# Kernel tuning notes

Measured on AMD Instinct MI355X. Metric: run time of the kernel, lower is better.

## Reference

```python
import jax, jax.numpy as jnp
import numpy as np

GAMMA = 0.1
EPS = 1e-10


def setup_inputs() -> dict:
    key = jax.random.key(0)
    ks = jax.random.split(key, 7)
    B, N, D = 1024, 2048, 128
    return {
        "target_embed": jax.random.normal(ks[0], (B, D), dtype=jnp.float32),
        "candidate_embeds": jax.random.normal(ks[1], (B, N, D), dtype=jnp.float32),
        "Wq": jax.random.normal(ks[2], (D, D), dtype=jnp.float32) * 0.05,
        "bq": jax.random.normal(ks[3], (D,), dtype=jnp.float32) * 0.05,
        "Wk": jax.random.normal(ks[4], (D, D), dtype=jnp.float32) * 0.05,
        "bk": jax.random.normal(ks[5], (D,), dtype=jnp.float32) * 0.05,
        "u": jax.random.uniform(ks[6], (B, N), dtype=jnp.float32),
        "num_neighbors": 32,
    }


def reference(target_embed, candidate_embeds, Wq, bq, Wk, bk, u, num_neighbors):
    B, N, D = candidate_embeds.shape
    scale = jnp.sqrt(jnp.float32(D))
    # Linear projections (torch Linear: x @ W.T + b)
    Q = target_embed @ Wq.T + bq                      # [B, D]
    K = jnp.einsum('bnd,ed->bne', candidate_embeds, Wk) + bk  # [B, N, D]
    scores = jnp.einsum('bd,bnd->bn', Q, K) / scale   # [B, N]
    p = jax.nn.softmax(scores, axis=-1)
    p = (1.0 - GAMMA) * p + GAMMA / N                 # mix with uniform
    # multinomial without replacement == Gumbel top-k on log-probs
    gumbel = -jnp.log(-jnp.log(u + EPS) + EPS)        # [B, N]
    _, sampled_idx = jax.lax.top_k(jnp.log(p) + gumbel, num_neighbors)  # [B, k]
    return sampled_idx
```

## Files before the change

### kernel.cpp

```cpp
#include <hip/hip_runtime.h>
#include <cmath>
#include <cfloat>
#include <climits>

constexpr int D    = 128;
constexpr float EPS_ = 1e-10f;
constexpr int KMAX = 64;

__global__ __launch_bounds__(128) void proj_kernel(
    const float* __restrict__ target, const float* __restrict__ Wq,
    const float* __restrict__ bq, const float* __restrict__ Wk,
    float* __restrict__ qt)
{
  __shared__ float sTgt[D];
  __shared__ float sQ[D];
  const int b = blockIdx.x, tid = threadIdx.x;
  sTgt[tid] = target[(size_t)b * D + tid];
  __syncthreads();
  float acc = 0.f;
  const float* wrow = Wq + (size_t)tid * D;
  #pragma unroll 8
  for (int e = 0; e < D; ++e) acc += sTgt[e] * wrow[e];
  sQ[tid] = acc + bq[tid];
  __syncthreads();
  acc = 0.f;
  #pragma unroll 8
  for (int d = 0; d < D; ++d) acc += sQ[d] * Wk[(size_t)d * D + tid];
  qt[(size_t)b * D + tid] = acc;
}

constexpr int NT1 = 256;
__global__ __launch_bounds__(NT1, 8) void score_kernel(
    const float* __restrict__ cand, const float* __restrict__ qt,
    float* __restrict__ scores, int N, int rows_per_blk)
{
  const int b    = blockIdx.x;
  const int tid  = threadIdx.x;
  const int lane = tid & 63;
  const int wave = tid >> 6;
  const int grp  = lane >> 4;
  const int gl   = lane & 15;

  const float* qp = qt + (size_t)b * D + gl * 8;
  float4 qa = ((const float4*)qp)[0];
  float4 qb = ((const float4*)qp)[1];

  const float scale = sqrtf((float)D);
  const int n0 = blockIdx.y * rows_per_blk;
  const int n1 = n0 + rows_per_blk;
  const float* base = cand + (size_t)b * N * D;
  float* srow = scores + (size_t)b * N;

  for (int n = n0 + wave * 4 + grp; n < n1; n += 32) {
    const float4* r0 = (const float4*)(base + (size_t)n * D);
    const float4* r1 = (const float4*)(base + (size_t)(n + 16) * D);
    float4 a0 = r0[gl * 2 + 0];
    float4 a1 = r0[gl * 2 + 1];
    float4 c0 = r1[gl * 2 + 0];
    float4 c1 = r1[gl * 2 + 1];
    float p0 = a0.x * qa.x + a0.y * qa.y + a0.z * qa.z + a0.w * qa.w
             + a1.x * qb.x + a1.y * qb.y + a1.z * qb.z + a1.w * qb.w;
    float p1 = c0.x * qa.x + c0.y * qa.y + c0.z * qa.z + c0.w * qa.w
             + c1.x * qb.x + c1.y * qb.y + c1.z * qb.z + c1.w * qb.w;
    p0 += __shfl_xor(p0, 1);  p1 += __shfl_xor(p1, 1);
    p0 += __shfl_xor(p0, 2);  p1 += __shfl_xor(p1, 2);
    p0 += __shfl_xor(p0, 4);  p1 += __shfl_xor(p1, 4);
    p0 += __shfl_xor(p0, 8);  p1 += __shfl_xor(p1, 8);
    if (gl == 0) { srow[n] = p0 / scale; srow[n + 16] = p1 / scale; }
  }
}

constexpr int NT2 = 256;
__global__ __launch_bounds__(NT2) void topk_kernel(
    const float* __restrict__ scores, const float* __restrict__ u,
    const int* __restrict__ kptr, int* __restrict__ out, int N)
{
  __shared__ float redM[4];
  __shared__ float redS[4];
  __shared__ float cV[4 * KMAX];
  __shared__ int   cI[4 * KMAX];

  const int b    = blockIdx.x;
  const int tid  = threadIdx.x;
  const int lane = tid & 63;
  const int wave = tid >> 6;
  const int base = wave * 512 + lane * 8;

  const float* srow = scores + (size_t)b * N;
  float4 s0 = ((const float4*)(srow + base))[0];
  float4 s1 = ((const float4*)(srow + base))[1];
  float v[8] = { s0.x, s0.y, s0.z, s0.w, s1.x, s1.y, s1.z, s1.w };

  float m = v[0];
  #pragma unroll
  for (int j = 1; j < 8; ++j) m = fmaxf(m, v[j]);
  for (int s = 32; s; s >>= 1) m = fmaxf(m, __shfl_xor(m, s));
  if (lane == 0) redM[wave] = m;
  __syncthreads();
  m = fmaxf(fmaxf(redM[0], redM[1]), fmaxf(redM[2], redM[3]));

  float ssum = 0.f;
  #pragma unroll
  for (int j = 0; j < 8; ++j) ssum += expf(v[j] - m);
  for (int s = 32; s; s >>= 1) ssum += __shfl_xor(ssum, s);
  if (lane == 0) redS[wave] = ssum;
  __syncthreads();
  const float Z = redS[0] + redS[1] + redS[2] + redS[3];

  const float mixc = (float)(0.1 / (double)N);
  const float* urow = u + (size_t)b * N;
  float4 u0 = ((const float4*)(urow + base))[0];
  float4 u1 = ((const float4*)(urow + base))[1];
  float uu[8] = { u0.x, u0.y, u0.z, u0.w, u1.x, u1.y, u1.z, u1.w };
  #pragma unroll
  for (int j = 0; j < 8; ++j) {
    float pmix = 0.9f * (expf(v[j] - m) / Z) + mixc;
    float g = -logf(-logf(uu[j] + EPS_) + EPS_);
    v[j] = logf(pmix) + g;
  }

  const int k = kptr[0];

  for (int i = 0; i < k; ++i) {
    float bv = v[0]; int bj = 0;
    #pragma unroll
    for (int j = 1; j < 8; ++j) if (v[j] > bv) { bv = v[j]; bj = j; }
    int bidx = base + bj;
    for (int s = 32; s; s >>= 1) {
      float ov = __shfl_xor(bv, s);
      int   oi = __shfl_xor(bidx, s);
      if (ov > bv || (ov == bv && oi < bidx)) { bv = ov; bidx = oi; }
    }
    if (lane == ((bidx - wave * 512) >> 3)) {
      int off = bidx & 7;
      #pragma unroll
      for (int j = 0; j < 8; ++j) if (off == j) v[j] = -FLT_MAX;
    }
    if (lane == 0) { cV[wave * KMAX + i] = bv; cI[wave * KMAX + i] = bidx; }
  }
  __syncthreads();

  if (wave == 0) {
    const int tot = 4 * k;
    float mv[4]; int mi[4];
    #pragma unroll
    for (int t = 0; t < 4; ++t) {
      int c = lane + 64 * t;
      if (c < tot) {
        int w = c / k, i = c % k;
        mv[t] = cV[w * KMAX + i]; mi[t] = cI[w * KMAX + i];
      } else { mv[t] = -FLT_MAX; mi[t] = INT_MAX; }
    }
    for (int i = 0; i < k; ++i) {
      float bv = mv[0]; int bidx = mi[0];
      #pragma unroll
      for (int t = 1; t < 4; ++t)
        if (mv[t] > bv || (mv[t] == bv && mi[t] < bidx)) { bv = mv[t]; bidx = mi[t]; }
      for (int s = 32; s; s >>= 1) {
        float ov = __shfl_xor(bv, s);
        int   oi = __shfl_xor(bidx, s);
        if (ov > bv || (ov == bv && oi < bidx)) { bv = ov; bidx = oi; }
      }
      #pragma unroll
      for (int t = 0; t < 4; ++t) if (mi[t] == bidx) mv[t] = -FLT_MAX;
      if (lane == 0) out[(size_t)b * k + i] = bidx;
    }
  }
}

constexpr int NTF = 512;
constexpr int NWF = NTF / 64;
__global__ __launch_bounds__(NTF, 8) void fused_kernel(
    const float* __restrict__ target, const float* __restrict__ cand,
    const float* __restrict__ Wq, const float* __restrict__ bq,
    const float* __restrict__ Wk, const float* __restrict__ u,
    const int* __restrict__ kptr, int* __restrict__ out, int N)
{
  extern __shared__ float sS[];
  __shared__ float sTgt[D];
  __shared__ float sQ[D];
  __shared__ float sQt[D];
  __shared__ float redV[NWF];
  __shared__ int   redI[NWF];

  const int b = blockIdx.x, tid = threadIdx.x;
  const int lane = tid & 63, wave = tid >> 6;

  if (tid < D) sTgt[tid] = target[(size_t)b * D + tid];
  __syncthreads();
  if (tid < D) {
    float acc = 0.f;
    const float* wrow = Wq + (size_t)tid * D;
    #pragma unroll 8
    for (int e = 0; e < D; ++e) acc += sTgt[e] * wrow[e];
    sQ[tid] = acc + bq[tid];
  }
  __syncthreads();
  if (tid < D) {
    float acc = 0.f;
    #pragma unroll 8
    for (int d = 0; d < D; ++d) acc += sQ[d] * Wk[(size_t)d * D + tid];
    sQt[tid] = acc;
  }
  __syncthreads();

  const int grp = lane >> 4, gl = lane & 15;
  float q0 = sQt[gl*8+0], q1 = sQt[gl*8+1], q2 = sQt[gl*8+2], q3 = sQt[gl*8+3];
  float q4 = sQt[gl*8+4], q5 = sQt[gl*8+5], q6 = sQt[gl*8+6], q7 = sQt[gl*8+7];
  const float scale = sqrtf((float)D);
  const int rstride = NWF * 4;
  int n = wave * 4 + grp;
  for (; n + rstride < N; n += 2 * rstride) {
    const float4* r0 = (const float4*)(cand + ((size_t)b * N + n) * D);
    const float4* r1 = (const float4*)(cand + ((size_t)b * N + n + rstride) * D);
    float4 a0 = r0[gl*2+0], a1 = r0[gl*2+1], c0 = r1[gl*2+0], c1 = r1[gl*2+1];
    float p0 = a0.x*q0 + a0.y*q1 + a0.z*q2 + a0.w*q3 + a1.x*q4 + a1.y*q5 + a1.z*q6 + a1.w*q7;
    float p1 = c0.x*q0 + c0.y*q1 + c0.z*q2 + c0.w*q3 + c1.x*q4 + c1.y*q5 + c1.z*q6 + c1.w*q7;
    p0 += __shfl_xor(p0,1); p1 += __shfl_xor(p1,1);
    p0 += __shfl_xor(p0,2); p1 += __shfl_xor(p1,2);
    p0 += __shfl_xor(p0,4); p1 += __shfl_xor(p1,4);
    p0 += __shfl_xor(p0,8); p1 += __shfl_xor(p1,8);
    if (gl == 0) { sS[n] = p0 / scale; sS[n + rstride] = p1 / scale; }
  }
  if (n < N) {
    const float4* r0 = (const float4*)(cand + ((size_t)b * N + n) * D);
    float4 a0 = r0[gl*2+0], a1 = r0[gl*2+1];
    float p0 = a0.x*q0 + a0.y*q1 + a0.z*q2 + a0.w*q3 + a1.x*q4 + a1.y*q5 + a1.z*q6 + a1.w*q7;
    p0 += __shfl_xor(p0,1); p0 += __shfl_xor(p0,2); p0 += __shfl_xor(p0,4); p0 += __shfl_xor(p0,8);
    if (gl == 0) sS[n] = p0 / scale;
  }
  __syncthreads();

  float m = -FLT_MAX;
  for (int i = tid; i < N; i += NTF) m = fmaxf(m, sS[i]);
  for (int s = 32; s; s >>= 1) m = fmaxf(m, __shfl_xor(m, s));
  if (lane == 0) redV[wave] = m;
  __syncthreads();
  m = redV[0];
  #pragma unroll
  for (int w = 1; w < NWF; ++w) m = fmaxf(m, redV[w]);
  __syncthreads();

  float ssum = 0.f;
  for (int i = tid; i < N; i += NTF) ssum += expf(sS[i] - m);
  for (int s = 32; s; s >>= 1) ssum += __shfl_xor(ssum, s);
  if (lane == 0) redV[wave] = ssum;
  __syncthreads();
  float Z = redV[0];
  #pragma unroll
  for (int w = 1; w < NWF; ++w) Z += redV[w];
  __syncthreads();

  const float mixc = (float)(0.1 / (double)N);
  for (int i = tid; i < N; i += NTF) {
    float pmix = 0.9f * (expf(sS[i] - m) / Z) + mixc;
    float uv = u[(size_t)b * N + i];
    float g = -logf(-logf(uv + EPS_) + EPS_);
    sS[i] = logf(pmix) + g;
  }
  __syncthreads();

  const int k = kptr[0];
  for (int i = 0; i < k; ++i) {
    float bv = -FLT_MAX; int bi = N;
    for (int j = tid; j < N; j += NTF) {
      float vv = sS[j];
      if (vv > bv || (vv == bv && j < bi)) { bv = vv; bi = j; }
    }
    for (int s = 32; s; s >>= 1) {
      float ov = __shfl_xor(bv, s); int oi = __shfl_xor(bi, s);
      if (ov > bv || (ov == bv && oi < bi)) { bv = ov; bi = oi; }
    }
    if (lane == 0) { redV[wave] = bv; redI[wave] = bi; }
    __syncthreads();
    if (tid == 0) {
      float fv = redV[0]; int fi = redI[0];
      #pragma unroll
      for (int w = 1; w < NWF; ++w)
        if (redV[w] > fv || (redV[w] == fv && redI[w] < fi)) { fv = redV[w]; fi = redI[w]; }
      out[(size_t)b * k + i] = fi;
      sS[fi] = -FLT_MAX;
    }
    __syncthreads();
  }
}

extern "C" void kernel_launch(void* const* d_in, const int* in_sizes, int n_in,
                              void* d_out, int out_size, void* d_ws, size_t ws_size,
                              hipStream_t stream) {
  const float* target = (const float*)d_in[0];
  const float* cand   = (const float*)d_in[1];
  const float* Wq     = (const float*)d_in[2];
  const float* bq     = (const float*)d_in[3];
  const float* Wk     = (const float*)d_in[4];
  const float* bk     = (const float*)d_in[5];
  const float* u      = (const float*)d_in[6];
  const int*   kptr   = (const int*)d_in[7];
  (void)bk; (void)n_in;

  const int B = in_sizes[0] / D;
  const int N = in_sizes[1] / (B * D);
  const int k = out_size / B;

  const size_t need = ((size_t)B * N + (size_t)B * D) * sizeof(float);
  const bool ok3 = (ws_size >= need) && (N == NT2 * 8) && (k <= KMAX) &&
                   (N % 128 == 0);

  if (ok3) {
    float* scores = (float*)d_ws;
    float* qt     = scores + (size_t)B * N;
    proj_kernel<<<B, 128, 0, stream>>>(target, Wq, bq, Wk, qt);
    const int chunks = 4;
    const int rows_per_blk = N / chunks;
    score_kernel<<<dim3(B, chunks), NT1, 0, stream>>>(cand, qt, scores, N, rows_per_blk);
    topk_kernel<<<B, NT2, 0, stream>>>(scores, u, kptr, (int*)d_out, N);
  } else {
    fused_kernel<<<B, NTF, N * sizeof(float), stream>>>(
        target, cand, Wq, bq, Wk, u, kptr, (int*)d_out, N);
  }
}
```

Before: 271.1 us.

## Fuse projection, scoring and top-k into one kernel per batch row

Replaces the three-kernel path (projection, score, top-k) with a single 512-thread kernel per batch row. Scores stay in shared memory instead of round-tripping through a global workspace, which removes two kernel launches and the score write and read-back. The candidate read now maps one float4 per lane with two rows per wave instruction. The cost is one block per row (1024 blocks) where scoring previously used four blocks per row, so there is less parallelism for the bandwidth-bound candidate stream. The projection also redoes the two 128x128 matvecs inside each block with only 128 of 512 threads active.

```diff
diff --git a/kernel.cpp b/kernel.cpp
--- a/kernel.cpp
+++ b/kernel.cpp
@@ -4,147 +4,141 @@
 #include <climits>
 
 constexpr int D    = 128;
+constexpr int NT   = 512;
+constexpr int NW   = NT / 64;
+constexpr int KMAX = 64;
 constexpr float EPS_ = 1e-10f;
-constexpr int KMAX = 64;
-
-__global__ __launch_bounds__(128) void proj_kernel(
-    const float* __restrict__ target, const float* __restrict__ Wq,
-    const float* __restrict__ bq, const float* __restrict__ Wk,
-    float* __restrict__ qt)
+
+__global__ __launch_bounds__(NT, 8) void fused2_kernel(
+    const float* __restrict__ target, const float* __restrict__ cand,
+    const float* __restrict__ Wq, const float* __restrict__ bq,
+    const float* __restrict__ Wk, const float* __restrict__ u,
+    const int* __restrict__ kptr, int* __restrict__ out, int N)
 {
-  __shared__ float sTgt[D];
-  __shared__ float sQ[D];
-  const int b = blockIdx.x, tid = threadIdx.x;
-  sTgt[tid] = target[(size_t)b * D + tid];
-  __syncthreads();
-  float acc = 0.f;
-  const float* wrow = Wq + (size_t)tid * D;
-  #pragma unroll 8
-  for (int e = 0; e < D; ++e) acc += sTgt[e] * wrow[e];
-  sQ[tid] = acc + bq[tid];
-  __syncthreads();
-  acc = 0.f;
-  #pragma unroll 8
-  for (int d = 0; d < D; ++d) acc += sQ[d] * Wk[(size_t)d * D + tid];
-  qt[(size_t)b * D + tid] = acc;
-}
-
-constexpr int NT1 = 256;
-__global__ __launch_bounds__(NT1, 8) void score_kernel(
-    const float* __restrict__ cand, const float* __restrict__ qt,
-    float* __restrict__ scores, int N, int rows_per_blk)
-{
+  extern __shared__ __align__(16) float sS[];
+  __shared__ __align__(16) float sTgt[D];
+  __shared__ __align__(16) float sQ[D];
+  __shared__ __align__(16) float sQt[D];
+  __shared__ float redM[NW];
+  __shared__ float cV[NW * KMAX];
+  __shared__ int   cI[NW * KMAX];
+
   const int b    = blockIdx.x;
   const int tid  = threadIdx.x;
   const int lane = tid & 63;
   const int wave = tid >> 6;
-  const int grp  = lane >> 4;
-  const int gl   = lane & 15;
-
-  const float* qp = qt + (size_t)b * D + gl * 8;
-  float4 qa = ((const float4*)qp)[0];
-  float4 qb = ((const float4*)qp)[1];
-
-  const float scale = sqrtf((float)D);
-  const int n0 = blockIdx.y * rows_per_blk;
-  const int n1 = n0 + rows_per_blk;
+
+  if (tid < D) sTgt[tid] = target[(size_t)b * D + tid];
+  __syncthreads();
+  if (tid < D) {
+    float acc = 0.f;
+    const float* wrow = Wq + (size_t)tid * D;
+    #pragma unroll 8
+    for (int e = 0; e < D; ++e) acc += sTgt[e] * wrow[e];
+    sQ[tid] = acc + bq[tid];
+  }
+  __syncthreads();
+  if (tid < D) {
+    float acc = 0.f;
+    #pragma unroll 8
+    for (int d = 0; d < D; ++d) acc += sQ[d] * Wk[(size_t)d * D + tid];
+    sQt[tid] = acc;
+  }
+  __syncthreads();
+
+  const int p    = lane & 31;
+  const int half = lane >> 5;
+  const float4 qf = ((const float4*)sQt)[p];
+  const float inv_scale = 1.0f / sqrtf((float)D);
   const float* base = cand + (size_t)b * N * D;
-  float* srow = scores + (size_t)b * N;
-
-  for (int n = n0 + wave * 4 + grp; n < n1; n += 32) {
-    const float4* r0 = (const float4*)(base + (size_t)n * D);
-    const float4* r1 = (const float4*)(base + (size_t)(n + 16) * D);
-    float4 a0 = r0[gl * 2 + 0];
-    float4 a1 = r0[gl * 2 + 1];
-    float4 c0 = r1[gl * 2 + 0];
-    float4 c1 = r1[gl * 2 + 1];
-    float p0 = a0.x * qa.x + a0.y * qa.y + a0.z * qa.z + a0.w * qa.w
-             + a1.x * qb.x + a1.y * qb.y + a1.z * qb.z + a1.w * qb.w;
-    float p1 = c0.x * qa.x + c0.y * qa.y + c0.z * qa.z + c0.w * qa.w
-             + c1.x * qb.x + c1.y * qb.y + c1.z * qb.z + c1.w * qb.w;
-    p0 += __shfl_xor(p0, 1);  p1 += __shfl_xor(p1, 1);
-    p0 += __shfl_xor(p0, 2);  p1 += __shfl_xor(p1, 2);
-    p0 += __shfl_xor(p0, 4);  p1 += __shfl_xor(p1, 4);
-    p0 += __shfl_xor(p0, 8);  p1 += __shfl_xor(p1, 8);
-    if (gl == 0) { srow[n] = p0 / scale; srow[n + 16] = p1 / scale; }
-  }
-}
-
-constexpr int NT2 = 256;
-__global__ __launch_bounds__(NT2) void topk_kernel(
-    const float* __restrict__ scores, const float* __restrict__ u,
-    const int* __restrict__ kptr, int* __restrict__ out, int N)
-{
-  __shared__ float redM[4];
-  __shared__ float redS[4];
-  __shared__ float cV[4 * KMAX];
-  __shared__ int   cI[4 * KMAX];
-
-  const int b    = blockIdx.x;
-  const int tid  = threadIdx.x;
-  const int lane = tid & 63;
-  const int wave = tid >> 6;
-  const int base = wave * 512 + lane * 8;
-
-  const float* srow = scores + (size_t)b * N;
-  float4 s0 = ((const float4*)(srow + base))[0];
-  float4 s1 = ((const float4*)(srow + base))[1];
-  float v[8] = { s0.x, s0.y, s0.z, s0.w, s1.x, s1.y, s1.z, s1.w };
-
-  float m = v[0];
-  #pragma unroll
-  for (int j = 1; j < 8; ++j) m = fmaxf(m, v[j]);
+
+  for (int n0 = wave * 8; n0 < N; n0 += NW * 8) {
+    const float4* r0 = (const float4*)(base + (size_t)(n0 + 0) * D) + lane;
+    const float4* r1 = (const float4*)(base + (size_t)(n0 + 2) * D) + lane;
+    const float4* r2 = (const float4*)(base + (size_t)(n0 + 4) * D) + lane;
+    const float4* r3 = (const float4*)(base + (size_t)(n0 + 6) * D) + lane;
+    float4 a0 = *r0, a1 = *r1, a2 = *r2, a3 = *r3;
+    float s0 = a0.x * qf.x + a0.y * qf.y + a0.z * qf.z + a0.w * qf.w;
+    float s1 = a1.x * qf.x + a1.y * qf.y + a1.z * qf.z + a1.w * qf.w;
+    float s2 = a2.x * qf.x + a2.y * qf.y + a2.z * qf.z + a2.w * qf.w;
+    float s3 = a3.x * qf.x + a3.y * qf.y + a3.z * qf.z + a3.w * qf.w;
+    s0 += __shfl_xor(s0, 1);  s1 += __shfl_xor(s1, 1);
+    s2 += __shfl_xor(s2, 1);  s3 += __shfl_xor(s3, 1);
+    s0 += __shfl_xor(s0, 2);  s1 += __shfl_xor(s1, 2);
+    s2 += __shfl_xor(s2, 2);  s3 += __shfl_xor(s3, 2);
+    s0 += __shfl_xor(s0, 4);  s1 += __shfl_xor(s1, 4);
+    s2 += __shfl_xor(s2, 4);  s3 += __shfl_xor(s3, 4);
+    s0 += __shfl_xor(s0, 8);  s1 += __shfl_xor(s1, 8);
+    s2 += __shfl_xor(s2, 8);  s3 += __shfl_xor(s3, 8);
+    s0 += __shfl_xor(s0, 16); s1 += __shfl_xor(s1, 16);
+    s2 += __shfl_xor(s2, 16); s3 += __shfl_xor(s3, 16);
+    if (p == 0) {
+      sS[n0 + 0 + half] = s0 * inv_scale;
+      sS[n0 + 2 + half] = s1 * inv_scale;
+      sS[n0 + 4 + half] = s2 * inv_scale;
+      sS[n0 + 6 + half] = s3 * inv_scale;
+    }
+  }
+  __syncthreads();
+
+  const int iv = wave * 256 + lane * 4;
+  float4 sv = *(const float4*)(sS + iv);
+  float v0 = sv.x, v1 = sv.y, v2 = sv.z, v3 = sv.w;
+
+  float m = fmaxf(fmaxf(v0, v1), fmaxf(v2, v3));
   for (int s = 32; s; s >>= 1) m = fmaxf(m, __shfl_xor(m, s));
   if (lane == 0) redM[wave] = m;
   __syncthreads();
-  m = fmaxf(fmaxf(redM[0], redM[1]), fmaxf(redM[2], redM[3]));
-
-  float ssum = 0.f;
+  m = redM[0];
   #pragma unroll
-  for (int j = 0; j < 8; ++j) ssum += expf(v[j] - m);
+  for (int w = 1; w < NW; ++w) m = fmaxf(m, redM[w]);
+  __syncthreads();
+
+  float ssum = expf(v0 - m) + expf(v1 - m) + expf(v2 - m) + expf(v3 - m);
   for (int s = 32; s; s >>= 1) ssum += __shfl_xor(ssum, s);
-  if (lane == 0) redS[wave] = ssum;
-  __syncthreads();
-  const float Z = redS[0] + redS[1] + redS[2] + redS[3];
+  if (lane == 0) redM[wave] = ssum;
+  __syncthreads();
+  float Z = redM[0];
+  #pragma unroll
+  for (int w = 1; w < NW; ++w) Z += redM[w];
+  __syncthreads();
 
   const float mixc = (float)(0.1 / (double)N);
-  const float* urow = u + (size_t)b * N;
-  float4 u0 = ((const float4*)(urow + base))[0];
-  float4 u1 = ((const float4*)(urow + base))[1];
-  float uu[8] = { u0.x, u0.y, u0.z, u0.w, u1.x, u1.y, u1.z, u1.w };
-  #pragma unroll
-  for (int j = 0; j < 8; ++j) {
-    float pmix = 0.9f * (expf(v[j] - m) / Z) + mixc;
-    float g = -logf(-logf(uu[j] + EPS_) + EPS_);
-    v[j] = logf(pmix) + g;
-  }
+  float4 uv = *(const float4*)(u + (size_t)b * N + iv);
+  v0 = logf(0.9f * (expf(v0 - m) / Z) + mixc) + (-logf(-logf(uv.x + EPS_) + EPS_));
+  v1 = logf(0.9f * (expf(v1 - m) / Z) + mixc) + (-logf(-logf(uv.y + EPS_) + EPS_));
+  v2 = logf(0.9f * (expf(v2 - m) / Z) + mixc) + (-logf(-logf(uv.z + EPS_) + EPS_));
+  v3 = logf(0.9f * (expf(v3 - m) / Z) + mixc) + (-logf(-logf(uv.w + EPS_) + EPS_));
 
   const int k = kptr[0];
 
   for (int i = 0; i < k; ++i) {
-    float bv = v[0]; int bj = 0;
-    #pragma unroll
-    for (int j = 1; j < 8; ++j) if (v[j] > bv) { bv = v[j]; bj = j; }
-    int bidx = base + bj;
+    float bv = v0; int bj = 0;
+    if (v1 > bv) { bv = v1; bj = 1; }
+    if (v2 > bv) { bv = v2; bj = 2; }
+    if (v3 > bv) { bv = v3; bj = 3; }
+    int bidx = iv + bj;
     for (int s = 32; s; s >>= 1) {
       float ov = __shfl_xor(bv, s);
       int   oi = __shfl_xor(bidx, s);
       if (ov > bv || (ov == bv && oi < bidx)) { bv = ov; bidx = oi; }
     }
-    if (lane == ((bidx - wave * 512) >> 3)) {
-      int off = bidx & 7;
-      #pragma unroll
-      for (int j = 0; j < 8; ++j) if (off == j) v[j] = -FLT_MAX;
+    if (lane == ((bidx & 255) >> 2)) {
+      int off = bidx & 3;
+      if (off == 0) v0 = -FLT_MAX;
+      if (off == 1) v1 = -FLT_MAX;
+      if (off == 2) v2 = -FLT_MAX;
+      if (off == 3) v3 = -FLT_MAX;
     }
     if (lane == 0) { cV[wave * KMAX + i] = bv; cI[wave * KMAX + i] = bidx; }
   }
   __syncthreads();
 
   if (wave == 0) {
-    const int tot = 4 * k;
-    float mv[4]; int mi[4];
+    const int tot = NW * k;
+    float mv[8]; int mi[8];
     #pragma unroll
-    for (int t = 0; t < 4; ++t) {
+    for (int t = 0; t < 8; ++t) {
       int c = lane + 64 * t;
       if (c < tot) {
         int w = c / k, i = c % k;
@@ -154,7 +148,7 @@
     for (int i = 0; i < k; ++i) {
       float bv = mv[0]; int bidx = mi[0];
       #pragma unroll
-      for (int t = 1; t < 4; ++t)
+      for (int t = 1; t < 8; ++t)
         if (mv[t] > bv || (mv[t] == bv && mi[t] < bidx)) { bv = mv[t]; bidx = mi[t]; }
       for (int s = 32; s; s >>= 1) {
         float ov = __shfl_xor(bv, s);
@@ -162,7 +156,7 @@
         if (ov > bv || (ov == bv && oi < bidx)) { bv = ov; bidx = oi; }
       }
       #pragma unroll
-      for (int t = 0; t < 4; ++t) if (mi[t] == bidx) mv[t] = -FLT_MAX;
+      for (int t = 0; t < 8; ++t) if (mi[t] == bidx) mv[t] = -FLT_MAX;
       if (lane == 0) out[(size_t)b * k + i] = bidx;
     }
   }
@@ -254,8 +248,8 @@
   const float mixc = (float)(0.1 / (double)N);
   for (int i = tid; i < N; i += NTF) {
     float pmix = 0.9f * (expf(sS[i] - m) / Z) + mixc;
-    float uv = u[(size_t)b * N + i];
-    float g = -logf(-logf(uv + EPS_) + EPS_);
+    float uvs = u[(size_t)b * N + i];
+    float g = -logf(-logf(uvs + EPS_) + EPS_);
     sS[i] = logf(pmix) + g;
   }
   __syncthreads();
@@ -296,24 +290,15 @@
   const float* bk     = (const float*)d_in[5];
   const float* u      = (const float*)d_in[6];
   const int*   kptr   = (const int*)d_in[7];
-  (void)bk; (void)n_in;
+  (void)bk; (void)n_in; (void)d_ws; (void)ws_size;
 
   const int B = in_sizes[0] / D;
   const int N = in_sizes[1] / (B * D);
   const int k = out_size / B;
 
-  const size_t need = ((size_t)B * N + (size_t)B * D) * sizeof(float);
-  const bool ok3 = (ws_size >= need) && (N == NT2 * 8) && (k <= KMAX) &&
-                   (N % 128 == 0);
-
-  if (ok3) {
-    float* scores = (float*)d_ws;
-    float* qt     = scores + (size_t)B * N;
-    proj_kernel<<<B, 128, 0, stream>>>(target, Wq, bq, Wk, qt);
-    const int chunks = 4;
-    const int rows_per_blk = N / chunks;
-    score_kernel<<<dim3(B, chunks), NT1, 0, stream>>>(cand, qt, scores, N, rows_per_blk);
-    topk_kernel<<<B, NT2, 0, stream>>>(scores, u, kptr, (int*)d_out, N);
+  if (N == NT * 4 && (N % 64) == 0 && k <= KMAX) {
+    fused2_kernel<<<B, NT, N * sizeof(float), stream>>>(
+        target, cand, Wq, bq, Wk, u, kptr, (int*)d_out, N);
   } else {
     fused_kernel<<<B, NTF, N * sizeof(float), stream>>>(
         target, cand, Wq, bq, Wk, u, kptr, (int*)d_out, N);
```

After: 246.3 us. 1.1x faster.

## Restructure score kernel with nontemporal loads, DPP reductions and double-buffered slots

Applied to the files above, without the earlier changes.

The score kernel now runs two blocks per batch row instead of four. Each wave processes 8-row slots, with each half-wave reducing one row through DPP row operations in place of shuffles. Candidate loads are nontemporal and double-buffered so the next slot's loads are in flight while the current one is reduced. A per-block rotation of the slot order spreads memory access. The aim is to stream the 1 GB candidate tensor closer to HBM bandwidth, at the cost of hardcoding N=2048, since the chunk and slot constants assume 1024 rows per block.

```diff
diff --git a/kernel.cpp b/kernel.cpp
--- a/kernel.cpp
+++ b/kernel.cpp
@@ -4,8 +4,28 @@
 #include <climits>
 
 constexpr int D    = 128;
+constexpr int KMAX = 64;
 constexpr float EPS_ = 1e-10f;
-constexpr int KMAX = 64;
+
+typedef float vf4 __attribute__((ext_vector_type(4)));
+__device__ __forceinline__ float4 ntload(const float4* p) {
+  vf4 v = __builtin_nontemporal_load((const vf4*)p);
+  return make_float4(v.x, v.y, v.z, v.w);
+}
+
+template <int CTRL>
+__device__ __forceinline__ float dpp_add(float x) {
+  int y = __builtin_amdgcn_update_dpp(0, __float_as_int(x), CTRL, 0xf, 0xf, false);
+  return x + __int_as_float(y);
+}
+__device__ __forceinline__ float dpp_sum32(float x) {
+  x = dpp_add<0x111>(x);
+  x = dpp_add<0x112>(x);
+  x = dpp_add<0x114>(x);
+  x = dpp_add<0x118>(x);
+  x = dpp_add<0x142>(x);
+  return x;
+}
 
 __global__ __launch_bounds__(128) void proj_kernel(
     const float* __restrict__ target, const float* __restrict__ Wq,
@@ -29,44 +49,75 @@
   qt[(size_t)b * D + tid] = acc;
 }
 
-constexpr int NT1 = 256;
-__global__ __launch_bounds__(NT1, 8) void score_kernel(
+__global__ __launch_bounds__(256) void score_kernel(
     const float* __restrict__ cand, const float* __restrict__ qt,
-    float* __restrict__ scores, int N, int rows_per_blk)
+    float* __restrict__ scores, int N)
 {
-  const int b    = blockIdx.x;
-  const int tid  = threadIdx.x;
-  const int lane = tid & 63;
-  const int wave = tid >> 6;
-  const int grp  = lane >> 4;
-  const int gl   = lane & 15;
-
-  const float* qp = qt + (size_t)b * D + gl * 8;
-  float4 qa = ((const float4*)qp)[0];
-  float4 qb = ((const float4*)qp)[1];
-
-  const float scale = sqrtf((float)D);
-  const int n0 = blockIdx.y * rows_per_blk;
-  const int n1 = n0 + rows_per_blk;
-  const float* base = cand + (size_t)b * N * D;
-  float* srow = scores + (size_t)b * N;
-
-  for (int n = n0 + wave * 4 + grp; n < n1; n += 32) {
-    const float4* r0 = (const float4*)(base + (size_t)n * D);
-    const float4* r1 = (const float4*)(base + (size_t)(n + 16) * D);
-    float4 a0 = r0[gl * 2 + 0];
-    float4 a1 = r0[gl * 2 + 1];
-    float4 c0 = r1[gl * 2 + 0];
-    float4 c1 = r1[gl * 2 + 1];
-    float p0 = a0.x * qa.x + a0.y * qa.y + a0.z * qa.z + a0.w * qa.w
-             + a1.x * qb.x + a1.y * qb.y + a1.z * qb.z + a1.w * qb.w;
-    float p1 = c0.x * qa.x + c0.y * qa.y + c0.z * qa.z + c0.w * qa.w
-             + c1.x * qb.x + c1.y * qb.y + c1.z * qb.z + c1.w * qb.w;
-    p0 += __shfl_xor(p0, 1);  p1 += __shfl_xor(p1, 1);
-    p0 += __shfl_xor(p0, 2);  p1 += __shfl_xor(p1, 2);
-    p0 += __shfl_xor(p0, 4);  p1 += __shfl_xor(p1, 4);
-    p0 += __shfl_xor(p0, 8);  p1 += __shfl_xor(p1, 8);
-    if (gl == 0) { srow[n] = p0 / scale; srow[n + 16] = p1 / scale; }
+  const int bid   = blockIdx.x;
+  const int b     = bid >> 1;
+  const int chunk = bid & 1;
+  const int tid   = threadIdx.x;
+  const int lane  = tid & 63;
+  const int wave  = tid >> 6;
+  const int p     = lane & 31;
+  const int half  = lane >> 5;
+
+  const float4 qf = ((const float4*)(qt + (size_t)b * D))[p];
+  const float inv_scale = 1.0f / sqrtf((float)D);
+
+  const float4* cb4 = (const float4*)(cand + (size_t)b * N * D) +
+                      (size_t)chunk * 1024 * 32;
+  float* srow = scores + (size_t)b * N + chunk * 1024;
+
+  constexpr int SLOTS = 128;
+  constexpr int ITERS = SLOTS / 4;
+  const int rot = (bid * 53) & (SLOTS - 1);
+
+  int slotA = (wave + rot) & (SLOTS - 1);
+  const float4* pA = cb4 + (size_t)slotA * 256 + lane;
+  float4 A0 = ntload(pA), A1 = ntload(pA + 64), A2 = ntload(pA + 128), A3 = ntload(pA + 192);
+
+  for (int i = 0; i < ITERS; i += 2) {
+    const int slotB = (wave + 4 * (i + 1) + rot) & (SLOTS - 1);
+    const float4* pB = cb4 + (size_t)slotB * 256 + lane;
+    float4 B0 = ntload(pB), B1 = ntload(pB + 64), B2 = ntload(pB + 128), B3 = ntload(pB + 192);
+
+    {
+      float s0 = A0.x * qf.x + A0.y * qf.y + A0.z * qf.z + A0.w * qf.w;
+      float s1 = A1.x * qf.x + A1.y * qf.y + A1.z * qf.z + A1.w * qf.w;
+      float s2 = A2.x * qf.x + A2.y * qf.y + A2.z * qf.z + A2.w * qf.w;
+      float s3 = A3.x * qf.x + A3.y * qf.y + A3.z * qf.z + A3.w * qf.w;
+      s0 = dpp_sum32(s0); s1 = dpp_sum32(s1); s2 = dpp_sum32(s2); s3 = dpp_sum32(s3);
+      if (p == 31) {
+        const int n0 = slotA * 8;
+        srow[n0 + 0 + half] = s0 * inv_scale;
+        srow[n0 + 2 + half] = s1 * inv_scale;
+        srow[n0 + 4 + half] = s2 * inv_scale;
+        srow[n0 + 6 + half] = s3 * inv_scale;
+      }
+    }
+
+    const int slotA2 = (wave + 4 * (i + 2) + rot) & (SLOTS - 1);
+    if (i + 2 < ITERS) {
+      const float4* pA2 = cb4 + (size_t)slotA2 * 256 + lane;
+      A0 = ntload(pA2); A1 = ntload(pA2 + 64); A2 = ntload(pA2 + 128); A3 = ntload(pA2 + 192);
+    }
+
+    {
+      float s0 = B0.x * qf.x + B0.y * qf.y + B0.z * qf.z + B0.w * qf.w;
+      float s1 = B1.x * qf.x + B1.y * qf.y + B1.z * qf.z + B1.w * qf.w;
+      float s2 = B2.x * qf.x + B2.y * qf.y + B2.z * qf.z + B2.w * qf.w;
+      float s3 = B3.x * qf.x + B3.y * qf.y + B3.z * qf.z + B3.w * qf.w;
+      s0 = dpp_sum32(s0); s1 = dpp_sum32(s1); s2 = dpp_sum32(s2); s3 = dpp_sum32(s3);
+      if (p == 31) {
+        const int n0 = slotB * 8;
+        srow[n0 + 0 + half] = s0 * inv_scale;
+        srow[n0 + 2 + half] = s1 * inv_scale;
+        srow[n0 + 4 + half] = s2 * inv_scale;
+        srow[n0 + 6 + half] = s3 * inv_scale;
+      }
+    }
+    slotA = slotA2;
   }
 }
 
@@ -254,8 +305,8 @@
   const float mixc = (float)(0.1 / (double)N);
   for (int i = tid; i < N; i += NTF) {
     float pmix = 0.9f * (expf(sS[i] - m) / Z) + mixc;
-    float uv = u[(size_t)b * N + i];
-    float g = -logf(-logf(uv + EPS_) + EPS_);
+    float uvs = u[(size_t)b * N + i];
+    float g = -logf(-logf(uvs + EPS_) + EPS_);
     sS[i] = logf(pmix) + g;
   }
   __syncthreads();
@@ -303,16 +354,13 @@
   const int k = out_size / B;
 
   const size_t need = ((size_t)B * N + (size_t)B * D) * sizeof(float);
-  const bool ok3 = (ws_size >= need) && (N == NT2 * 8) && (k <= KMAX) &&
-                   (N % 128 == 0);
+  const bool ok3 = (ws_size >= need) && (N == NT2 * 8) && (k <= KMAX);
 
   if (ok3) {
     float* scores = (float*)d_ws;
     float* qt     = scores + (size_t)B * N;
     proj_kernel<<<B, 128, 0, stream>>>(target, Wq, bq, Wk, qt);
-    const int chunks = 4;
-    const int rows_per_blk = N / chunks;
-    score_kernel<<<dim3(B, chunks), NT1, 0, stream>>>(cand, qt, scores, N, rows_per_blk);
+    score_kernel<<<B * 2, 256, 0, stream>>>(cand, qt, scores, N);
     topk_kernel<<<B, NT2, 0, stream>>>(scores, u, kptr, (int*)d_out, N);
   } else {
     fused_kernel<<<B, NTF, N * sizeof(float), stream>>>(
```

New measurement: 244.2 us. 9.9% less time.
